# Performance work log

Hardware: AMD Instinct MI355X
Metric: run time of the kernel (lower is better)

Reference implementation:

```python
import jax, jax.numpy as jnp
import numpy as np
from jax import lax


def _conv1d(x, w, b):
    # x: [B, C_in, L], w: [C_out, C_in, 3], 'same' padding
    y = lax.conv_general_dilated(x, w, window_strides=(1,), padding=[(1, 1)],
                                 dimension_numbers=('NCH', 'OIH', 'NCH'))
    return y + b[None, :, None]


def _bn(x, g, beta, mean, var, eps=1e-5):
    # BatchNorm1d in inference mode (running stats)
    scale = (g / jnp.sqrt(var + eps))[None, :, None]
    return (x - mean[None, :, None]) * scale + beta[None, :, None]


def setup_inputs() -> dict:
    key = jax.random.key(0)
    ks = jax.random.split(key, 24)
    B, L, C = 16, 8192, 256
    d = {}
    d['x'] = jax.random.normal(ks[0], (B, 1, L), dtype=jnp.float32)
    d['sc'] = 4
    d['fs'] = 16000
    # conv_fw_1: Conv1d(1, 256)
    d['w_in'] = jax.random.normal(ks[1], (C, 1, 3), dtype=jnp.float32) * 0.05
    d['b_in'] = jax.random.normal(ks[2], (C,), dtype=jnp.float32) * 0.05
    d['w_r1'] = jax.random.normal(ks[3], (C, C, 3), dtype=jnp.float32) * 0.02
    d['b_r1'] = jax.random.normal(ks[4], (C,), dtype=jnp.float32) * 0.05
    d['g1'] = 1.0 + 0.1 * jax.random.normal(ks[5], (C,), dtype=jnp.float32)
    d['be1'] = jax.random.normal(ks[6], (C,), dtype=jnp.float32) * 0.05
    d['m1'] = jax.random.normal(ks[7], (C,), dtype=jnp.float32) * 0.05
    d['v1'] = jax.random.uniform(ks[8], (C,), dtype=jnp.float32, minval=0.5, maxval=1.5)
    d['w_r2'] = jax.random.normal(ks[9], (C, C, 3), dtype=jnp.float32) * 0.02
    d['b_r2'] = jax.random.normal(ks[10], (C,), dtype=jnp.float32) * 0.05
    d['g2'] = 1.0 + 0.1 * jax.random.normal(ks[11], (C,), dtype=jnp.float32)
    d['be2'] = jax.random.normal(ks[12], (C,), dtype=jnp.float32) * 0.05
    d['m2'] = jax.random.normal(ks[13], (C,), dtype=jnp.float32) * 0.05
    d['v2'] = jax.random.uniform(ks[14], (C,), dtype=jnp.float32, minval=0.5, maxval=1.5)
    # up_sample: up_block1 Conv1d(256,256), up_block22 Conv1d(256,4)
    d['w_u1'] = jax.random.normal(ks[15], (C, C, 3), dtype=jnp.float32) * 0.02
    d['b_u1'] = jax.random.normal(ks[16], (C,), dtype=jnp.float32) * 0.05
    d['w_u2'] = jax.random.normal(ks[17], (4, C, 3), dtype=jnp.float32) * 0.02
    d['b_u2'] = jax.random.normal(ks[18], (4,), dtype=jnp.float32) * 0.05
    return d


def reference(x, sc, fs, w_in, b_in, w_r1, b_r1, g1, be1, m1, v1,
              w_r2, b_r2, g2, be2, m2, v2, w_u1, b_u1, w_u2, b_u2):
    SCALE = 0.15  # residual scale used in FDRN.forward
    R = 4         # FDRN.forward hard-codes Up(x, 4)
    h = jax.nn.relu(_conv1d(x, w_in, b_in))  # [B,256,L]

    def resblock(h):
        r = _bn(_conv1d(h, w_r1, b_r1), g1, be1, m1, v1)
        r = jax.nn.relu(r)
        r = _bn(_conv1d(r, w_r2, b_r2), g2, be2, m2, v2)
        return h + r * SCALE

    # same Resblock module applied 32 times (shared weights)
    h = lax.fori_loop(0, 32, lambda i, hh: resblock(hh), h)

    h = jax.nn.relu(_conv1d(h, w_u1, b_u1))   # [B,256,L]
    h = jax.nn.relu(_conv1d(h, w_u2, b_u2))   # [B,4,L]
    # _pharse_shift(I, r): New[i,0,j] = I[i, j % r, j // r]  ==  transpose + reshape
    B, C, L = h.shape
    h = jnp.transpose(h, (0, 2, 1)).reshape(B, 1, L * C)  # C == R == 4
    return jax.nn.relu(h)
```

## Files before the change

### kernel.cpp

```cpp
#include <hip/hip_runtime.h>

typedef _Float16 half8 __attribute__((ext_vector_type(8)));
typedef _Float16 half4 __attribute__((ext_vector_type(4)));
typedef __fp16 fp16x2 __attribute__((ext_vector_type(2)));
typedef float floatx4 __attribute__((ext_vector_type(4)));
typedef unsigned int uintx4 __attribute__((ext_vector_type(4)));

#define CCH 256
#define LSEQ 8192
#define LTILE 128
#define AROWS 132
#define NT 64
#define ROWB 512
#define LDSB (AROWS * ROWB)

__device__ __forceinline__ int swz(int row, int byte) {
  return row * ROWB + (byte ^ ((row & 7) << 4));
}
__device__ __forceinline__ floatx4 zero4() {
  floatx4 v; v[0] = 0.f; v[1] = 0.f; v[2] = 0.f; v[3] = 0.f; return v;
}
__device__ __forceinline__ unsigned long long pack4(float y0, float y1, float y2, float y3) {
  fp16x2 lo = __builtin_amdgcn_cvt_pkrtz(y0, y1);
  fp16x2 hi = __builtin_amdgcn_cvt_pkrtz(y2, y3);
  unsigned ulo = __builtin_bit_cast(unsigned, lo);
  unsigned uhi = __builtin_bit_cast(unsigned, hi);
  return (unsigned long long)ulo | ((unsigned long long)uhi << 32);
}

template <int MODE>
__global__ __launch_bounds__(512, 1) void res7(
    const _Float16* __restrict__ src, _Float16* __restrict__ dst,
    const _Float16* __restrict__ wA, const _Float16* __restrict__ wB,
    const float* __restrict__ sc1v, const float* __restrict__ sh1v,
    const float* __restrict__ sc2pv, const float* __restrict__ rs2v,
    const float* __restrict__ tshv) {
  __shared__ __align__(16) char smem[LDSB];
  const int t = threadIdx.x;
  const int bx = blockIdx.x;
  const int b = bx >> 6;
  const int tile = bx & (NT - 1);
  const int l0 = tile * LTILE;

  for (int c = t; c < AROWS * 32; c += 512) {
    const int row = c >> 5, col = c & 31;
    const int l = l0 + row - 2;
    uintx4 v = {0u, 0u, 0u, 0u};
    if (l >= 0 && l < LSEQ)
      v = *(const uintx4*)(src + (((size_t)b * LSEQ + l) << 8) + col * 8);
    *(uintx4*)(smem + swz(row, col * 16)) = v;
  }
  __syncthreads();

  const int w = t >> 6, ln = t & 63;
  const int cg = w >> 1, lgrp = w & 1;
  const int lrow = ln & 15, kgrp = ln >> 4;
  const size_t wbase = (size_t)(cg * 64 + lrow) * 32 + kgrp * 8;

  if constexpr (MODE == 0) {
    const int jtb = lgrp * 5;
    const int njt = lgrp ? 4 : 5;
    floatx4 acc[4][5];
#pragma unroll
    for (int i = 0; i < 4; ++i)
#pragma unroll
      for (int j = 0; j < 5; ++j) acc[i][j] = zero4();
    {
      const _Float16* wp = wA + wbase;
      half8 a0 = *(const half8*)(wp);
      half8 a1 = *(const half8*)(wp + 16 * 32);
      half8 a2 = *(const half8*)(wp + 32 * 32);
      half8 a3 = *(const half8*)(wp + 48 * 32);
      for (int it = 0; it < 24; ++it) {
        const int nit = (it < 23) ? it + 1 : it;
        const _Float16* np = wA + (size_t)nit * (CCH * 32) + wbase;
        half8 n0 = *(const half8*)(np);
        half8 n1 = *(const half8*)(np + 16 * 32);
        half8 n2 = *(const half8*)(np + 32 * 32);
        half8 n3 = *(const half8*)(np + 48 * 32);
        const int tap = it >> 3, kc = it & 7;
        const int byt = kc * 64 + kgrp * 16;
        __builtin_amdgcn_s_setprio(1);
#pragma unroll
        for (int jj = 0; jj < 5; ++jj) {
          if (jj < njt) {
            int arow = (jtb + jj) * 16 + lrow + tap;
            if (arow > AROWS - 1) arow = AROWS - 1;
            half8 bf = *(const half8*)(smem + swz(arow, byt));
            acc[0][jj] = __builtin_amdgcn_mfma_f32_16x16x32_f16(a0, bf, acc[0][jj], 0, 0, 0);
            acc[1][jj] = __builtin_amdgcn_mfma_f32_16x16x32_f16(a1, bf, acc[1][jj], 0, 0, 0);
            acc[2][jj] = __builtin_amdgcn_mfma_f32_16x16x32_f16(a2, bf, acc[2][jj], 0, 0, 0);
            acc[3][jj] = __builtin_amdgcn_mfma_f32_16x16x32_f16(a3, bf, acc[3][jj], 0, 0, 0);
          }
        }
        __builtin_amdgcn_s_setprio(0);
        a0 = n0; a1 = n1; a2 = n2; a3 = n3;
      }
    }
    unsigned long long pk1[4][5];
#pragma unroll
    for (int i = 0; i < 4; ++i) {
      const int co = cg * 64 + i * 16 + kgrp * 4;
      floatx4 s = *(const floatx4*)(sc1v + co);
      floatx4 sh = *(const floatx4*)(sh1v + co);
#pragma unroll
      for (int jj = 0; jj < 5; ++jj) {
        if (jj < njt) {
          const int r = (jtb + jj) * 16 + lrow;
          if (r < 130) {
            const int l = l0 - 1 + r;
            const float m = ((l >= 0) && (l < LSEQ)) ? 1.f : 0.f;
            pk1[i][jj] = pack4(
                fmaxf(acc[i][jj][0] * s[0] + sh[0], 0.f) * m,
                fmaxf(acc[i][jj][1] * s[1] + sh[1], 0.f) * m,
                fmaxf(acc[i][jj][2] * s[2] + sh[2], 0.f) * m,
                fmaxf(acc[i][jj][3] * s[3] + sh[3], 0.f) * m);
          }
        }
      }
    }
    floatx4 c2[4][4];
#pragma unroll
    for (int i = 0; i < 4; ++i) {
      const int co = cg * 64 + i * 16 + kgrp * 4;
      floatx4 rs = *(const floatx4*)(rs2v + co);
      floatx4 ts = *(const floatx4*)(tshv + co);
#pragma unroll
      for (int j = 0; j < 4; ++j) {
        const int v = (lgrp * 4 + j) * 16 + lrow;
        half4 h = *(const half4*)(smem + swz(v + 2, co * 2));
#pragma unroll
        for (int q = 0; q < 4; ++q)
          c2[i][j][q] = (float)h[q] * rs[q] + ts[q];
      }
    }
    __syncthreads();
#pragma unroll
    for (int i = 0; i < 4; ++i) {
      const int co = cg * 64 + i * 16 + kgrp * 4;
#pragma unroll
      for (int jj = 0; jj < 5; ++jj) {
        if (jj < njt) {
          const int r = (jtb + jj) * 16 + lrow;
          if (r < 130)
            *(unsigned long long*)(smem + swz(r, co * 2)) = pk1[i][jj];
        }
      }
    }
    __syncthreads();
    {
      const _Float16* wp = wB + wbase;
      half8 a0 = *(const half8*)(wp);
      half8 a1 = *(const half8*)(wp + 16 * 32);
      half8 a2 = *(const half8*)(wp + 32 * 32);
      half8 a3 = *(const half8*)(wp + 48 * 32);
      for (int it = 0; it < 24; ++it) {
        const int nit = (it < 23) ? it + 1 : it;
        const _Float16* np = wB + (size_t)nit * (CCH * 32) + wbase;
        half8 n0 = *(const half8*)(np);
        half8 n1 = *(const half8*)(np + 16 * 32);
        half8 n2 = *(const half8*)(np + 32 * 32);
        half8 n3 = *(const half8*)(np + 48 * 32);
        const int tap = it >> 3, kc = it & 7;
        const int byt = kc * 64 + kgrp * 16;
        __builtin_amdgcn_s_setprio(1);
#pragma unroll
        for (int j = 0; j < 4; ++j) {
          const int brow = (lgrp * 4 + j) * 16 + lrow + tap;
          half8 bf = *(const half8*)(smem + swz(brow, byt));
          c2[0][j] = __builtin_amdgcn_mfma_f32_16x16x32_f16(a0, bf, c2[0][j], 0, 0, 0);
          c2[1][j] = __builtin_amdgcn_mfma_f32_16x16x32_f16(a1, bf, c2[1][j], 0, 0, 0);
          c2[2][j] = __builtin_amdgcn_mfma_f32_16x16x32_f16(a2, bf, c2[2][j], 0, 0, 0);
          c2[3][j] = __builtin_amdgcn_mfma_f32_16x16x32_f16(a3, bf, c2[3][j], 0, 0, 0);
        }
        __builtin_amdgcn_s_setprio(0);
        a0 = n0; a1 = n1; a2 = n2; a3 = n3;
      }
    }
#pragma unroll
    for (int i = 0; i < 4; ++i) {
      const int co = cg * 64 + i * 16 + kgrp * 4;
      floatx4 sp = *(const floatx4*)(sc2pv + co);
#pragma unroll
      for (int j = 0; j < 4; ++j) {
        const int v = (lgrp * 4 + j) * 16 + lrow;
        const int l = l0 + v;
        const size_t off = (((size_t)b * LSEQ + l) << 8) + co;
        half4 o;
#pragma unroll
        for (int q = 0; q < 4; ++q)
          o[q] = (_Float16)(c2[i][j][q] * sp[q]);
        *(half4*)(dst + off) = o;
      }
    }
  } else {
    floatx4 acc[4][4];
#pragma unroll
    for (int i = 0; i < 4; ++i)
#pragma unroll
      for (int j = 0; j < 4; ++j) acc[i][j] = zero4();
    for (int it = 0; it < 24; ++it) {
      const int tap = it >> 3, kc = it & 7;
      const _Float16* wp = wA + (size_t)it * (CCH * 32) + wbase;
      half8 a0 = *(const half8*)(wp);
      half8 a1 = *(const half8*)(wp + 16 * 32);
      half8 a2 = *(const half8*)(wp + 32 * 32);
      half8 a3 = *(const half8*)(wp + 48 * 32);
      const int byt = kc * 64 + kgrp * 16;
#pragma unroll
      for (int j = 0; j < 4; ++j) {
        const int arow = (lgrp * 4 + j) * 16 + lrow + 1 + tap;
        half8 bf = *(const half8*)(smem + swz(arow, byt));
        acc[0][j] = __builtin_amdgcn_mfma_f32_16x16x32_f16(a0, bf, acc[0][j], 0, 0, 0);
        acc[1][j] = __builtin_amdgcn_mfma_f32_16x16x32_f16(a1, bf, acc[1][j], 0, 0, 0);
        acc[2][j] = __builtin_amdgcn_mfma_f32_16x16x32_f16(a2, bf, acc[2][j], 0, 0, 0);
        acc[3][j] = __builtin_amdgcn_mfma_f32_16x16x32_f16(a3, bf, acc[3][j], 0, 0, 0);
      }
    }
#pragma unroll
    for (int i = 0; i < 4; ++i) {
      const int co = cg * 64 + i * 16 + kgrp * 4;
      floatx4 s = *(const floatx4*)(sc1v + co);
      floatx4 sh = *(const floatx4*)(sh1v + co);
#pragma unroll
      for (int j = 0; j < 4; ++j) {
        const int v = (lgrp * 4 + j) * 16 + lrow;
        const int l = l0 + v;
        unsigned long long pk = pack4(
            fmaxf(acc[i][j][0] * s[0] + sh[0], 0.f),
            fmaxf(acc[i][j][1] * s[1] + sh[1], 0.f),
            fmaxf(acc[i][j][2] * s[2] + sh[2], 0.f),
            fmaxf(acc[i][j][3] * s[3] + sh[3], 0.f));
        *(unsigned long long*)(dst + (((size_t)b * LSEQ + l) << 8) + co) = pk;
      }
    }
  }
}

__global__ void conv_in_kernel(const float* __restrict__ x, const float* __restrict__ w_in,
                               const float* __restrict__ b_in, _Float16* __restrict__ hout) {
  size_t idx = (size_t)blockIdx.x * blockDim.x + threadIdx.x;
  int co = (int)(idx & 255);
  size_t pos = idx >> 8;
  int l = (int)(pos & (LSEQ - 1));
  int b = (int)(pos >> 13);
  float acc = b_in[co];
#pragma unroll
  for (int k = 0; k < 3; ++k) {
    int lg = l + k - 1;
    if (lg >= 0 && lg < LSEQ) acc += w_in[co * 3 + k] * x[(size_t)b * LSEQ + lg];
  }
  hout[idx] = (_Float16)fmaxf(acc, 0.f);
}

__global__ __launch_bounds__(256) void conv_u2_kernel(
    const _Float16* __restrict__ hin, const float* __restrict__ w2T4 ,
    const float* __restrict__ b_u2, float* __restrict__ out) {
  const size_t idx = (size_t)blockIdx.x * 256 + threadIdx.x;
  const int l = (int)(idx & (LSEQ - 1));
  const int b = (int)(idx >> 13);
  floatx4 acc = *(const floatx4*)b_u2;
  for (int tap = 0; tap < 3; ++tap) {
    const int lg = l + tap - 1;
    if (lg < 0 || lg >= LSEQ) continue;
    const half8* hp = (const half8*)(hin + (((size_t)b * LSEQ + lg) << 8));
    const floatx4* wp = (const floatx4*)(w2T4 + tap * 1024);
    for (int q = 0; q < 32; ++q) {
      half8 hv = hp[q];
#pragma unroll
      for (int r = 0; r < 8; ++r) {
        floatx4 wv = wp[q * 8 + r];
        float h = (float)hv[r];
        acc[0] += h * wv[0]; acc[1] += h * wv[1]; acc[2] += h * wv[2]; acc[3] += h * wv[3];
      }
    }
  }
  floatx4 y;
#pragma unroll
  for (int r = 0; r < 4; ++r) y[r] = fmaxf(acc[r], 0.f);
  *(floatx4*)(out + ((size_t)b << 15) + (size_t)l * 4) = y;
}

__global__ void prep_kernel(
    const float* __restrict__ w_r1, const float* __restrict__ w_r2,
    const float* __restrict__ w_u1, const float* __restrict__ w_u2,
    const float* __restrict__ b_r1, const float* __restrict__ g1,
    const float* __restrict__ be1, const float* __restrict__ m1, const float* __restrict__ v1,
    const float* __restrict__ b_r2, const float* __restrict__ g2,
    const float* __restrict__ be2, const float* __restrict__ m2, const float* __restrict__ v2,
    const float* __restrict__ b_u1,
    _Float16* __restrict__ wT1, _Float16* __restrict__ wT2, _Float16* __restrict__ wTu1,
    float* __restrict__ wu2T4,
    float* __restrict__ sc1, float* __restrict__ sh1,
    float* __restrict__ sc2p, float* __restrict__ rs2, float* __restrict__ tsh,
    float* __restrict__ scu1, float* __restrict__ shu1) {
  int idx = blockIdx.x * blockDim.x + threadIdx.x;
  if (idx < 3 * CCH * CCH) {
    int tap = idx >> 16;
    int rem = idx & 65535;
    int kc = rem >> 13;
    int rem2 = rem & 8191;
    int co = rem2 >> 5, c = rem2 & 31;
    int ci = kc * 32 + c;
    size_t s = ((size_t)co * CCH + ci) * 3 + tap;
    wT1[idx] = (_Float16)w_r1[s];
    wT2[idx] = (_Float16)w_r2[s];
    wTu1[idx] = (_Float16)w_u1[s];
  }
  if (idx < 3 * CCH * 4) {
    int co = idx & 3;
    int ci = (idx >> 2) & 255;
    int tap = idx >> 10;
    wu2T4[idx] = w_u2[((size_t)co * CCH + ci) * 3 + tap];
  }
  if (idx < CCH) {
    float s1 = g1[idx] * rsqrtf(v1[idx] + 1e-5f);
    sc1[idx] = s1;
    sh1[idx] = (b_r1[idx] - m1[idx]) * s1 + be1[idx];
    float s2 = g2[idx] * rsqrtf(v2[idx] + 1e-5f);
    float sh2 = (b_r2[idx] - m2[idx]) * s2 + be2[idx];
    float sp = 0.15f * s2;
    sc2p[idx] = sp;
    rs2[idx] = 1.0f / sp;
    tsh[idx] = sh2 / s2;
    scu1[idx] = 1.f;
    shu1[idx] = b_u1[idx];
  }
}

__global__ void diag_kernel(float* out, float v) { out[0] = v; }

extern "C" void kernel_launch(void* const* d_in, const int* in_sizes, int n_in,
                              void* d_out, int out_size, void* d_ws, size_t ws_size,
                              hipStream_t stream) {
  (void)in_sizes; (void)n_in; (void)out_size;
  const size_t HELEMS = (size_t)16 * LSEQ * CCH;
  const size_t HB = HELEMS * sizeof(_Float16);
  const size_t NEED = 2 * HB + 2u * 1024 * 1024;
  if (ws_size < NEED) {
    diag_kernel<<<1, 1, 0, stream>>>((float*)d_out, 1000.0f + (float)(ws_size >> 20));
    return;
  }
  const float* x    = (const float*)d_in[0];
  const float* w_in = (const float*)d_in[3];
  const float* b_in = (const float*)d_in[4];
  const float* w_r1 = (const float*)d_in[5];
  const float* b_r1 = (const float*)d_in[6];
  const float* g1   = (const float*)d_in[7];
  const float* be1  = (const float*)d_in[8];
  const float* m1   = (const float*)d_in[9];
  const float* v1   = (const float*)d_in[10];
  const float* w_r2 = (const float*)d_in[11];
  const float* b_r2 = (const float*)d_in[12];
  const float* g2   = (const float*)d_in[13];
  const float* be2  = (const float*)d_in[14];
  const float* m2   = (const float*)d_in[15];
  const float* v2   = (const float*)d_in[16];
  const float* w_u1 = (const float*)d_in[17];
  const float* b_u1 = (const float*)d_in[18];
  const float* w_u2 = (const float*)d_in[19];
  const float* b_u2 = (const float*)d_in[20];

  char* ws = (char*)d_ws;
  _Float16* buf0 = (_Float16*)ws;
  _Float16* buf1 = (_Float16*)(ws + HB);
  _Float16* wT1  = (_Float16*)(ws + 2 * HB);
  _Float16* wT2  = wT1 + 3 * CCH * CCH;
  _Float16* wTu1 = wT2 + 3 * CCH * CCH;
  float* sc1  = (float*)(wTu1 + 3 * CCH * CCH);
  float* sh1  = sc1 + CCH;
  float* sc2p = sh1 + CCH;
  float* rs2  = sc2p + CCH;
  float* tsh  = rs2 + CCH;
  float* scu1 = tsh + CCH;
  float* shu1 = scu1 + CCH;
  float* wu2T4 = shu1 + CCH;

  prep_kernel<<<768, 256, 0, stream>>>(w_r1, w_r2, w_u1, w_u2, b_r1, g1, be1, m1, v1,
                                       b_r2, g2, be2, m2, v2, b_u1,
                                       wT1, wT2, wTu1, wu2T4, sc1, sh1, sc2p, rs2, tsh,
                                       scu1, shu1);
  conv_in_kernel<<<131072, 256, 0, stream>>>(x, w_in, b_in, buf0);
  const int grid = 16 * NT;
  for (int k = 0; k < 32; ++k) {
    const _Float16* s = (k & 1) ? buf1 : buf0;
    _Float16* d = (k & 1) ? buf0 : buf1;
    res7<0><<<grid, 512, 0, stream>>>(s, d, wT1, wT2, sc1, sh1, sc2p, rs2, tsh);
  }
  res7<1><<<grid, 512, 0, stream>>>(buf0, buf1, wTu1, (const _Float16*)nullptr,
                                    scu1, shu1, (const float*)nullptr,
                                    (const float*)nullptr, (const float*)nullptr);
  conv_u2_kernel<<<512, 256, 0, stream>>>(buf1, wu2T4, b_u2, (float*)d_out);
}
```

Before: 4.375 ms.

## Fuse two residual blocks per launch using wider halo recompute

Each kernel launch now applies two residual blocks back to back on a tile held in LDS, with the halo widened from 2 to 4 rows so the second block can be computed without a global round trip. This halves the number of launches and the global read/write traffic of the activation buffer across the 32 iterations. In exchange, each block computes 144 rows instead of the 132-row window it used before, so there is some redundant MFMA work on halo rows. The intermediate residual is also stored in fp16 in LDS between the two blocks, which matches the precision of the global buffer. An unused helper stub is left in the source.

Measured after the change: 4.596 ms. 5.1% more time.

```diff
diff --git a/kernel.cpp b/kernel.cpp
--- a/kernel.cpp
+++ b/kernel.cpp
@@ -9,7 +9,8 @@
 #define CCH 256
 #define LSEQ 8192
 #define LTILE 128
-#define AROWS 132
+#define HALO 4
+#define AROWS 136
 #define NT 64
 #define ROWB 512
 #define LDSB (AROWS * ROWB)
@@ -28,8 +29,56 @@
   return (unsigned long long)ulo | ((unsigned long long)uhi << 32);
 }
 
+template <int NJT, bool CLO, bool CHI>
+__device__ __forceinline__ void conv_mfma2(
+    const _Float16* __restrict__ wsrc, size_t wbase, const char* smem,
+    int jtb, int lrow, int kgrp, floatx4 (&acc)[5]) {
+  const _Float16* wp = wsrc + wbase;
+  half8 a0 = *(const half8*)(wp);
+  half8 a1 = *(const half8*)(wp + 16 * 32);
+  half8 a2 = *(const half8*)(wp + 32 * 32);
+  half8 a3 = *(const half8*)(wp + 48 * 32);
+  (void)a0;
+  (void)acc;
+}
+
+template <int NJT, bool CLO, bool CHI>
+__device__ __forceinline__ void conv_full(
+    const _Float16* __restrict__ wsrc, size_t wbase, const char* smem,
+    int jtb, int lrow, int kgrp, floatx4 (&acc)[4][5]) {
+  const _Float16* wp = wsrc + wbase;
+  half8 a0 = *(const half8*)(wp);
+  half8 a1 = *(const half8*)(wp + 16 * 32);
+  half8 a2 = *(const half8*)(wp + 32 * 32);
+  half8 a3 = *(const half8*)(wp + 48 * 32);
+  for (int it = 0; it < 24; ++it) {
+    const int nit = (it < 23) ? it + 1 : it;
+    const _Float16* np = wsrc + (size_t)nit * (CCH * 32) + wbase;
+    half8 n0 = *(const half8*)(np);
+    half8 n1 = *(const half8*)(np + 16 * 32);
+    half8 n2 = *(const half8*)(np + 32 * 32);
+    half8 n3 = *(const half8*)(np + 48 * 32);
+    const int tap = it >> 3, kc = it & 7;
+    const int byt = kc * 64 + kgrp * 16;
+    __builtin_amdgcn_s_setprio(1);
+#pragma unroll
+    for (int jj = 0; jj < NJT; ++jj) {
+      int row = (jtb + jj) * 16 + lrow + tap - 1;
+      if (CLO && jj == 0) row = row < 0 ? 0 : row;
+      if (CHI && jj == NJT - 1) row = row > AROWS - 1 ? AROWS - 1 : row;
+      half8 bf = *(const half8*)(smem + swz(row, byt));
+      acc[0][jj] = __builtin_amdgcn_mfma_f32_16x16x32_f16(a0, bf, acc[0][jj], 0, 0, 0);
+      acc[1][jj] = __builtin_amdgcn_mfma_f32_16x16x32_f16(a1, bf, acc[1][jj], 0, 0, 0);
+      acc[2][jj] = __builtin_amdgcn_mfma_f32_16x16x32_f16(a2, bf, acc[2][jj], 0, 0, 0);
+      acc[3][jj] = __builtin_amdgcn_mfma_f32_16x16x32_f16(a3, bf, acc[3][jj], 0, 0, 0);
+    }
+    __builtin_amdgcn_s_setprio(0);
+    a0 = n0; a1 = n1; a2 = n2; a3 = n3;
+  }
+}
+
 template <int MODE>
-__global__ __launch_bounds__(512, 1) void res7(
+__global__ __launch_bounds__(512, 1) void res9(
     const _Float16* __restrict__ src, _Float16* __restrict__ dst,
     const _Float16* __restrict__ wA, const _Float16* __restrict__ wB,
     const float* __restrict__ sc1v, const float* __restrict__ sh1v,
@@ -44,7 +93,7 @@
 
   for (int c = t; c < AROWS * 32; c += 512) {
     const int row = c >> 5, col = c & 31;
-    const int l = l0 + row - 2;
+    const int l = l0 + row - HALO;
     uintx4 v = {0u, 0u, 0u, 0u};
     if (l >= 0 && l < LSEQ)
       v = *(const uintx4*)(src + (((size_t)b * LSEQ + l) << 8) + col * 8);
@@ -58,13 +107,120 @@
   const size_t wbase = (size_t)(cg * 64 + lrow) * 32 + kgrp * 8;
 
   if constexpr (MODE == 0) {
-    const int jtb = lgrp * 5;
+    const int jtb = lgrp ? 5 : 0;
     const int njt = lgrp ? 4 : 5;
-    floatx4 acc[4][5];
+    for (int rb = 0; rb < 2; ++rb) {
+      const int wlo1 = 1 + 2 * rb, whi1 = 135 - 2 * rb;
+      const int wlo2 = 2 + 2 * rb, whi2 = 134 - 2 * rb;
+      floatx4 acc[4][5];
+#pragma unroll
+      for (int i = 0; i < 4; ++i)
+#pragma unroll
+        for (int j = 0; j < 5; ++j) acc[i][j] = zero4();
+      if (lgrp == 0) conv_full<5, true, false>(wA, wbase, smem, 0, lrow, kgrp, acc);
+      else           conv_full<4, false, true>(wA, wbase, smem, 5, lrow, kgrp, acc);
+      unsigned long long pk1[4][5];
+#pragma unroll
+      for (int i = 0; i < 4; ++i) {
+        const int co = cg * 64 + i * 16 + kgrp * 4;
+        floatx4 s = *(const floatx4*)(sc1v + co);
+        floatx4 sh = *(const floatx4*)(sh1v + co);
+#pragma unroll
+        for (int jj = 0; jj < 5; ++jj) {
+          if (jj < njt) {
+            const int wr = (jtb + jj) * 16 + lrow;
+            const int l = l0 - HALO + wr;
+            const float m = (wr >= wlo1 && wr < whi1 && l >= 0 && l < LSEQ) ? 1.f : 0.f;
+            pk1[i][jj] = pack4(
+                fmaxf(acc[i][jj][0] * s[0] + sh[0], 0.f) * m,
+                fmaxf(acc[i][jj][1] * s[1] + sh[1], 0.f) * m,
+                fmaxf(acc[i][jj][2] * s[2] + sh[2], 0.f) * m,
+                fmaxf(acc[i][jj][3] * s[3] + sh[3], 0.f) * m);
+          }
+        }
+      }
+      floatx4 c2[4][5];
+#pragma unroll
+      for (int i = 0; i < 4; ++i) {
+        const int co = cg * 64 + i * 16 + kgrp * 4;
+        floatx4 rs = *(const floatx4*)(rs2v + co);
+        floatx4 ts = *(const floatx4*)(tshv + co);
+#pragma unroll
+        for (int jj = 0; jj < 5; ++jj) {
+          if (jj < njt) {
+            int wr = (jtb + jj) * 16 + lrow;
+            if (wr > AROWS - 1) wr = AROWS - 1;
+            half4 h = *(const half4*)(smem + swz(wr, co * 2));
+#pragma unroll
+            for (int q = 0; q < 4; ++q)
+              c2[i][jj][q] = (float)h[q] * rs[q] + ts[q];
+          }
+        }
+      }
+      __syncthreads();
+#pragma unroll
+      for (int i = 0; i < 4; ++i) {
+        const int co = cg * 64 + i * 16 + kgrp * 4;
+#pragma unroll
+        for (int jj = 0; jj < 5; ++jj) {
+          if (jj < njt) {
+            const int wr = (jtb + jj) * 16 + lrow;
+            if (wr < AROWS)
+              *(unsigned long long*)(smem + swz(wr, co * 2)) = pk1[i][jj];
+          }
+        }
+      }
+      __syncthreads();
+      if (lgrp == 0) conv_full<5, true, false>(wB, wbase, smem, 0, lrow, kgrp, c2);
+      else           conv_full<4, false, true>(wB, wbase, smem, 5, lrow, kgrp, c2);
+      if (rb == 0) {
+#pragma unroll
+        for (int i = 0; i < 4; ++i) {
+          const int co = cg * 64 + i * 16 + kgrp * 4;
+          floatx4 sp = *(const floatx4*)(sc2pv + co);
+#pragma unroll
+          for (int jj = 0; jj < 5; ++jj) {
+            if (jj < njt) {
+              const int wr = (jtb + jj) * 16 + lrow;
+              const int l = l0 - HALO + wr;
+              const float m = (wr >= wlo2 && wr < whi2 && l >= 0 && l < LSEQ) ? 1.f : 0.f;
+              unsigned long long pk = pack4(
+                  c2[i][jj][0] * sp[0] * m, c2[i][jj][1] * sp[1] * m,
+                  c2[i][jj][2] * sp[2] * m, c2[i][jj][3] * sp[3] * m);
+              if (wr < AROWS)
+                *(unsigned long long*)(smem + swz(wr, co * 2)) = pk;
+            }
+          }
+        }
+        __syncthreads();
+      } else {
+#pragma unroll
+        for (int i = 0; i < 4; ++i) {
+          const int co = cg * 64 + i * 16 + kgrp * 4;
+          floatx4 sp = *(const floatx4*)(sc2pv + co);
+#pragma unroll
+          for (int jj = 0; jj < 5; ++jj) {
+            if (jj < njt) {
+              const int wr = (jtb + jj) * 16 + lrow;
+              if (wr >= 4 && wr < 132) {
+                const int l = l0 - HALO + wr;
+                const size_t off = (((size_t)b * LSEQ + l) << 8) + co;
+                unsigned long long pk = pack4(
+                    c2[i][jj][0] * sp[0], c2[i][jj][1] * sp[1],
+                    c2[i][jj][2] * sp[2], c2[i][jj][3] * sp[3]);
+                *(unsigned long long*)(dst + off) = pk;
+              }
+            }
+          }
+        }
+      }
+    }
+  } else {
+    floatx4 acc[4][4];
 #pragma unroll
     for (int i = 0; i < 4; ++i)
 #pragma unroll
-      for (int j = 0; j < 5; ++j) acc[i][j] = zero4();
+      for (int j = 0; j < 4; ++j) acc[i][j] = zero4();
     {
       const _Float16* wp = wA + wbase;
       half8 a0 = *(const half8*)(wp);
@@ -82,150 +238,26 @@
         const int byt = kc * 64 + kgrp * 16;
         __builtin_amdgcn_s_setprio(1);
 #pragma unroll
-        for (int jj = 0; jj < 5; ++jj) {
-          if (jj < njt) {
-            int arow = (jtb + jj) * 16 + lrow + tap;
-            if (arow > AROWS - 1) arow = AROWS - 1;
-            half8 bf = *(const half8*)(smem + swz(arow, byt));
-            acc[0][jj] = __builtin_amdgcn_mfma_f32_16x16x32_f16(a0, bf, acc[0][jj], 0, 0, 0);
-            acc[1][jj] = __builtin_amdgcn_mfma_f32_16x16x32_f16(a1, bf, acc[1][jj], 0, 0, 0);
-            acc[2][jj] = __builtin_amdgcn_mfma_f32_16x16x32_f16(a2, bf, acc[2][jj], 0, 0, 0);
-            acc[3][jj] = __builtin_amdgcn_mfma_f32_16x16x32_f16(a3, bf, acc[3][jj], 0, 0, 0);
-          }
+        for (int j = 0; j < 4; ++j) {
+          const int row = (lgrp * 4 + j) * 16 + lrow + 3 + tap;
+          half8 bf = *(const half8*)(smem + swz(row, byt));
+          acc[0][j] = __builtin_amdgcn_mfma_f32_16x16x32_f16(a0, bf, acc[0][j], 0, 0, 0);
+          acc[1][j] = __builtin_amdgcn_mfma_f32_16x16x32_f16(a1, bf, acc[1][j], 0, 0, 0);
+          acc[2][j] = __builtin_amdgcn_mfma_f32_16x16x32_f16(a2, bf, acc[2][j], 0, 0, 0);
+          acc[3][j] = __builtin_amdgcn_mfma_f32_16x16x32_f16(a3, bf, acc[3][j], 0, 0, 0);
         }
         __builtin_amdgcn_s_setprio(0);
         a0 = n0; a1 = n1; a2 = n2; a3 = n3;
       }
     }
-    unsigned long long pk1[4][5];
 #pragma unroll
     for (int i = 0; i < 4; ++i) {
       const int co = cg * 64 + i * 16 + kgrp * 4;
       floatx4 s = *(const floatx4*)(sc1v + co);
       floatx4 sh = *(const floatx4*)(sh1v + co);
 #pragma unroll
-      for (int jj = 0; jj < 5; ++jj) {
-        if (jj < njt) {
-          const int r = (jtb + jj) * 16 + lrow;
-          if (r < 130) {
-            const int l = l0 - 1 + r;
-            const float m = ((l >= 0) && (l < LSEQ)) ? 1.f : 0.f;
-            pk1[i][jj] = pack4(
-                fmaxf(acc[i][jj][0] * s[0] + sh[0], 0.f) * m,
-                fmaxf(acc[i][jj][1] * s[1] + sh[1], 0.f) * m,
-                fmaxf(acc[i][jj][2] * s[2] + sh[2], 0.f) * m,
-                fmaxf(acc[i][jj][3] * s[3] + sh[3], 0.f) * m);
-          }
-        }
-      }
-    }
-    floatx4 c2[4][4];
-#pragma unroll
-    for (int i = 0; i < 4; ++i) {
-      const int co = cg * 64 + i * 16 + kgrp * 4;
-      floatx4 rs = *(const floatx4*)(rs2v + co);
-      floatx4 ts = *(const floatx4*)(tshv + co);
-#pragma unroll
       for (int j = 0; j < 4; ++j) {
-        const int v = (lgrp * 4 + j) * 16 + lrow;
-        half4 h = *(const half4*)(smem + swz(v + 2, co * 2));
-#pragma unroll
-        for (int q = 0; q < 4; ++q)
-          c2[i][j][q] = (float)h[q] * rs[q] + ts[q];
-      }
-    }
-    __syncthreads();
-#pragma unroll
-    for (int i = 0; i < 4; ++i) {
-      const int co = cg * 64 + i * 16 + kgrp * 4;
-#pragma unroll
-      for (int jj = 0; jj < 5; ++jj) {
-        if (jj < njt) {
-          const int r = (jtb + jj) * 16 + lrow;
-          if (r < 130)
-            *(unsigned long long*)(smem + swz(r, co * 2)) = pk1[i][jj];
-        }
-      }
-    }
-    __syncthreads();
-    {
-      const _Float16* wp = wB + wbase;
-      half8 a0 = *(const half8*)(wp);
-      half8 a1 = *(const half8*)(wp + 16 * 32);
-      half8 a2 = *(const half8*)(wp + 32 * 32);
-      half8 a3 = *(const half8*)(wp + 48 * 32);
-      for (int it = 0; it < 24; ++it) {
-        const int nit = (it < 23) ? it + 1 : it;
-        const _Float16* np = wB + (size_t)nit * (CCH * 32) + wbase;
-        half8 n0 = *(const half8*)(np);
-        half8 n1 = *(const half8*)(np + 16 * 32);
-        half8 n2 = *(const half8*)(np + 32 * 32);
-        half8 n3 = *(const half8*)(np + 48 * 32);
-        const int tap = it >> 3, kc = it & 7;
-        const int byt = kc * 64 + kgrp * 16;
-        __builtin_amdgcn_s_setprio(1);
-#pragma unroll
-        for (int j = 0; j < 4; ++j) {
-          const int brow = (lgrp * 4 + j) * 16 + lrow + tap;
-          half8 bf = *(const half8*)(smem + swz(brow, byt));
-          c2[0][j] = __builtin_amdgcn_mfma_f32_16x16x32_f16(a0, bf, c2[0][j], 0, 0, 0);
-          c2[1][j] = __builtin_amdgcn_mfma_f32_16x16x32_f16(a1, bf, c2[1][j], 0, 0, 0);
-          c2[2][j] = __builtin_amdgcn_mfma_f32_16x16x32_f16(a2, bf, c2[2][j], 0, 0, 0);
-          c2[3][j] = __builtin_amdgcn_mfma_f32_16x16x32_f16(a3, bf, c2[3][j], 0, 0, 0);
-        }
-        __builtin_amdgcn_s_setprio(0);
-        a0 = n0; a1 = n1; a2 = n2; a3 = n3;
-      }
-    }
-#pragma unroll
-    for (int i = 0; i < 4; ++i) {
-      const int co = cg * 64 + i * 16 + kgrp * 4;
-      floatx4 sp = *(const floatx4*)(sc2pv + co);
-#pragma unroll
-      for (int j = 0; j < 4; ++j) {
-        const int v = (lgrp * 4 + j) * 16 + lrow;
-        const int l = l0 + v;
-        const size_t off = (((size_t)b * LSEQ + l) << 8) + co;
-        half4 o;
-#pragma unroll
-        for (int q = 0; q < 4; ++q)
-          o[q] = (_Float16)(c2[i][j][q] * sp[q]);
-        *(half4*)(dst + off) = o;
-      }
-    }
-  } else {
-    floatx4 acc[4][4];
-#pragma unroll
-    for (int i = 0; i < 4; ++i)
-#pragma unroll
-      for (int j = 0; j < 4; ++j) acc[i][j] = zero4();
-    for (int it = 0; it < 24; ++it) {
-      const int tap = it >> 3, kc = it & 7;
-      const _Float16* wp = wA + (size_t)it * (CCH * 32) + wbase;
-      half8 a0 = *(const half8*)(wp);
-      half8 a1 = *(const half8*)(wp + 16 * 32);
-      half8 a2 = *(const half8*)(wp + 32 * 32);
-      half8 a3 = *(const half8*)(wp + 48 * 32);
-      const int byt = kc * 64 + kgrp * 16;
-#pragma unroll
-      for (int j = 0; j < 4; ++j) {
-        const int arow = (lgrp * 4 + j) * 16 + lrow + 1 + tap;
-        half8 bf = *(const half8*)(smem + swz(arow, byt));
-        acc[0][j] = __builtin_amdgcn_mfma_f32_16x16x32_f16(a0, bf, acc[0][j], 0, 0, 0);
-        acc[1][j] = __builtin_amdgcn_mfma_f32_16x16x32_f16(a1, bf, acc[1][j], 0, 0, 0);
-        acc[2][j] = __builtin_amdgcn_mfma_f32_16x16x32_f16(a2, bf, acc[2][j], 0, 0, 0);
-        acc[3][j] = __builtin_amdgcn_mfma_f32_16x16x32_f16(a3, bf, acc[3][j], 0, 0, 0);
-      }
-    }
-#pragma unroll
-    for (int i = 0; i < 4; ++i) {
-      const int co = cg * 64 + i * 16 + kgrp * 4;
-      floatx4 s = *(const floatx4*)(sc1v + co);
-      floatx4 sh = *(const floatx4*)(sh1v + co);
-#pragma unroll
-      for (int j = 0; j < 4; ++j) {
-        const int v = (lgrp * 4 + j) * 16 + lrow;
-        const int l = l0 + v;
+        const int l = l0 + (lgrp * 4 + j) * 16 + lrow;
         unsigned long long pk = pack4(
             fmaxf(acc[i][j][0] * s[0] + sh[0], 0.f),
             fmaxf(acc[i][j][1] * s[1] + sh[1], 0.f),
@@ -382,12 +414,12 @@
                                        scu1, shu1);
   conv_in_kernel<<<131072, 256, 0, stream>>>(x, w_in, b_in, buf0);
   const int grid = 16 * NT;
-  for (int k = 0; k < 32; ++k) {
+  for (int k = 0; k < 16; ++k) {
     const _Float16* s = (k & 1) ? buf1 : buf0;
     _Float16* d = (k & 1) ? buf0 : buf1;
-    res7<0><<<grid, 512, 0, stream>>>(s, d, wT1, wT2, sc1, sh1, sc2p, rs2, tsh);
-  }
-  res7<1><<<grid, 512, 0, stream>>>(buf0, buf1, wTu1, (const _Float16*)nullptr,
+    res9<0><<<grid, 512, 0, stream>>>(s, d, wT1, wT2, sc1, sh1, sc2p, rs2, tsh);
+  }
+  res9<1><<<grid, 512, 0, stream>>>(buf0, buf1, wTu1, (const _Float16*)nullptr,
                                     scu1, shu1, (const float*)nullptr,
                                     (const float*)nullptr, (const float*)nullptr);
   conv_u2_kernel<<<512, 256, 0, stream>>>(buf1, wu2T4, b_u2, (float*)d_out);
```
